# Optimization experiments

Hardware: AMD Instinct MI355X
Metric: run time of the kernel (lower is better)

The kernel has to match this reference:

```python
import jax, jax.numpy as jnp
import numpy as np

EMBED_DIM = 1024
NUM_HEADS = 16
HEAD_DIM = EMBED_DIM // NUM_HEADS
SCALE = HEAD_DIM ** -0.5


def setup_inputs() -> dict:
    key = jax.random.key(0)
    k_x, k_qkv, k_w, k_b = jax.random.split(key, 4)
    B, N = 2, 2048
    x = jax.random.normal(k_x, (B, N, EMBED_DIM), dtype=jnp.float32)
    # nn.Linear weights stored as (out, in); init with small normal
    w_qkv = jax.random.normal(k_qkv, (3 * EMBED_DIM, EMBED_DIM), dtype=jnp.float32) * (EMBED_DIM ** -0.5)
    w_out = jax.random.normal(k_w, (EMBED_DIM, EMBED_DIM), dtype=jnp.float32) * (EMBED_DIM ** -0.5)
    b_out = jax.random.normal(k_b, (EMBED_DIM,), dtype=jnp.float32) * 0.02
    return {"x": x, "w_qkv": w_qkv, "w_out": w_out, "b_out": b_out}


def reference(x, w_qkv, w_out, b_out):
    B, N, _ = x.shape
    # qkv: (B, N, 3*E) -> (B, N, 3, H, Dh)
    qkv = jnp.einsum('bne,fe->bnf', x, w_qkv).reshape(B, N, 3, NUM_HEADS, HEAD_DIM)
    q, k, v = qkv[:, :, 0], qkv[:, :, 1], qkv[:, :, 2]
    scores = jnp.einsum('bnhd,bmhd->bhnm', q, k) * SCALE
    attn = jax.nn.softmax(scores, axis=-1)  # dropout is identity in eval mode
    out = jnp.einsum('bhnm,bmhd->bnhd', attn, v).reshape(B, N, EMBED_DIM)
    return jnp.einsum('bne,fe->bnf', out, w_out) + b_out
```

## Files before the change

### kernel.cpp

```cpp
#include <hip/hip_runtime.h>
#include <stdint.h>
#include <stddef.h>

#define SEQ   2048
#define BATCH 2
#define NTOK  (SEQ*BATCH)
#define EMB   1024
#define QKVN  3072
#define NH    16
#define HD    64

typedef __bf16 bf16x8 __attribute__((ext_vector_type(8)));
typedef float  f32x4  __attribute__((ext_vector_type(4)));

__device__ __forceinline__ unsigned short f2b(float f) {
  union { float f; uint32_t u; } v; v.f = f;
  uint32_t r = v.u + 0x7fffu + ((v.u >> 16) & 1u);
  return (unsigned short)(r >> 16);
}

#define GLOAD_LDS16(gp, lp)                                                    \
  __builtin_amdgcn_global_load_lds(                                            \
      (__attribute__((address_space(1))) void*)(gp),                           \
      (__attribute__((address_space(3))) void*)(lp), 16, 0, 0)

__global__ void cvt3_kernel(const float* __restrict__ x,
                            const float* __restrict__ wq,
                            const float* __restrict__ wo,
                            unsigned short* __restrict__ xb,
                            unsigned short* __restrict__ wqb,
                            unsigned short* __restrict__ wob) {
  int i = blockIdx.x * blockDim.x + threadIdx.x;
  const float* in; unsigned short* out; int k;
  if (i < 1048576)              { in = x;  out = xb;  k = i; }
  else if (i < 1048576+786432)  { in = wq; out = wqb; k = i - 1048576; }
  else                          { in = wo; out = wob; k = i - (1048576+786432); }
  float4 v = ((const float4*)in)[k];
  ushort4 o;
  o.x = f2b(v.x); o.y = f2b(v.y); o.z = f2b(v.z); o.w = f2b(v.w);
  ((ushort4*)out)[k] = o;
}

__global__ __launch_bounds__(256) void gemm_bt(
    const unsigned short* __restrict__ A,
    const unsigned short* __restrict__ B,
    unsigned short* __restrict__ Cb,
    float* __restrict__ Cf,
    const float* __restrict__ bias,
    unsigned short* __restrict__ vt,
    int M, int N, int K, int mode)
{
  __shared__ unsigned short As[128*64];
  __shared__ unsigned short Bs[128*64];

  const int tid  = threadIdx.x;
  const int wave = tid >> 6, lane = tid & 63;
  const int l16  = lane & 15, quad = lane >> 4;
  const int tm = blockIdx.x * 128, tn = blockIdx.y * 128;
  const int wm = (wave & 1) * 64,  wn = (wave >> 1) * 64;

  f32x4 acc[4][4] = {};

  for (int k0 = 0; k0 < K; k0 += 64) {
    __syncthreads();
#pragma unroll
    for (int j = 0; j < 4; ++j) {
      const int p   = (wave*4 + j)*64 + lane;
      const int row = p >> 3;
      const int c   = ((p & 7) ^ (row & 7)) << 3;
      GLOAD_LDS16(A + (size_t)(tm + row)*K + (k0 + c), As + (wave*4 + j)*512);
      GLOAD_LDS16(B + (size_t)(tn + row)*K + (k0 + c), Bs + (wave*4 + j)*512);
    }
    __syncthreads();

#pragma unroll
    for (int ks = 0; ks < 2; ++ks) {
      bf16x8 af[4], bf[4];
#pragma unroll
      for (int i = 0; i < 4; ++i) {
        const int ca = ((ks*4 + quad) ^ (l16 & 7)) << 3;
        af[i] = *(const bf16x8*)(As + (wm + i*16 + l16)*64 + ca);
        bf[i] = *(const bf16x8*)(Bs + (wn + i*16 + l16)*64 + ca);
      }
#pragma unroll
      for (int mi = 0; mi < 4; ++mi)
#pragma unroll
        for (int ni = 0; ni < 4; ++ni)
          acc[mi][ni] = __builtin_amdgcn_mfma_f32_16x16x32_bf16(af[mi], bf[ni], acc[mi][ni], 0, 0, 0);
    }
  }

  if (mode == 1) {
#pragma unroll
    for (int mi = 0; mi < 4; ++mi)
#pragma unroll
      for (int ni = 0; ni < 4; ++ni)
#pragma unroll
        for (int r = 0; r < 4; ++r) {
          const int row = tm + wm + mi*16 + quad*4 + r;
          const int col = tn + wn + ni*16 + l16;
          Cf[(size_t)row*N + col] = acc[mi][ni][r] + bias[col];
        }
  } else {
    if (tn < 2048) {
#pragma unroll
      for (int mi = 0; mi < 4; ++mi)
#pragma unroll
        for (int ni = 0; ni < 4; ++ni)
#pragma unroll
          for (int r = 0; r < 4; ++r) {
            const int row = tm + wm + mi*16 + quad*4 + r;
            const int col = tn + wn + ni*16 + l16;
            Cb[(size_t)row*2048 + col] = f2b(acc[mi][ni][r]);
          }
    } else {
#pragma unroll
      for (int mi = 0; mi < 4; ++mi)
#pragma unroll
        for (int ni = 0; ni < 4; ++ni) {
          const int f    = tn + wn + ni*16 + l16 - 2048;
          const int row0 = tm + wm + mi*16 + quad*4;
          const int bb   = row0 >> 11;
          const int n0   = row0 & 2047;
          ushort4 pv;
          pv.x = f2b(acc[mi][ni][0]); pv.y = f2b(acc[mi][ni][1]);
          pv.z = f2b(acc[mi][ni][2]); pv.w = f2b(acc[mi][ni][3]);
          *(ushort4*)(vt + ((size_t)(bb*1024 + f))*2048 + n0) = pv;
        }
    }
  }
}

__global__ __launch_bounds__(256) void attn_kernel(
    const unsigned short* __restrict__ qk,
    const unsigned short* __restrict__ vT,
    unsigned short* __restrict__ aout)
{
  __shared__ unsigned short Ks[2][64*64];
  __shared__ unsigned short Vt[2][64*64];
  __shared__ unsigned short Pl[4*16*64];

  const int tid  = threadIdx.x;
  const int wave = tid >> 6, lane = tid & 63;
  const int l16  = lane & 15, quad = lane >> 4;

  const int flat = blockIdx.x;
  const int xcd  = flat & 7;
  const int idx  = flat >> 3;
  const int bh   = xcd*4 + (idx >> 5);
  const int qt   = idx & 31;
  const int b  = bh >> 4, h = bh & 15;
  const size_t tok0 = (size_t)b * SEQ;
  const int qrow0 = qt*64 + wave*16;
  const int swz = (l16 & 7) << 3;

  const int sp0  = wave*64 + lane;
  const int sp1  = 256 + wave*64 + lane;
  const int srow0 = sp0 >> 3, sc0 = ((sp0 & 7) ^ (srow0 & 7)) << 3;
  const int srow1 = sp1 >> 3, sc1 = ((sp1 & 7) ^ (srow1 & 7)) << 3;
  const unsigned short* kbase = qk + tok0*2048 + 1024 + h*64;
  const unsigned short* vbase = vT + ((size_t)(b*1024 + h*64))*2048;
  const int ldst0 = (wave*64)*8;
  const int ldst1 = (256 + wave*64)*8;

#define STAGE(dst, kk0s)                                                      \
  do {                                                                        \
    GLOAD_LDS16(kbase + (size_t)((kk0s) + srow0)*2048 + sc0, Ks[dst] + ldst0);\
    GLOAD_LDS16(vbase + (size_t)srow0*2048 + (kk0s) + sc0,   Vt[dst] + ldst0);\
    GLOAD_LDS16(kbase + (size_t)((kk0s) + srow1)*2048 + sc1, Ks[dst] + ldst1);\
    GLOAD_LDS16(vbase + (size_t)srow1*2048 + (kk0s) + sc1,   Vt[dst] + ldst1);\
  } while (0)

  bf16x8 qf[2];
  {
    const unsigned short* qp = qk + (tok0 + qrow0 + l16)*2048 + h*64;
#pragma unroll
    for (int ks = 0; ks < 2; ++ks) {
      bf16x8 t = *(const bf16x8*)(qp + ks*32 + quad*8);
#pragma unroll
      for (int j = 0; j < 8; ++j) t[j] = (__bf16)((float)t[j] * 0.125f);
      qf[ks] = t;
    }
  }

  f32x4 oacc[4] = {};
  float l_run = 0.f;
  unsigned short* Pw = Pl + wave*(16*64);
  const float LOG2E = 1.44269504f;
  const float OFF2  = 17.3123405f;

  STAGE(0, 0);
  __syncthreads();

  for (int kb = 0; kb < SEQ/64; ++kb) {
    const int cur = kb & 1;
    if (kb + 1 < SEQ/64) STAGE(cur ^ 1, (kb + 1)*64);

    const unsigned short* Kc = Ks[cur];
    const unsigned short* Vc = Vt[cur];

    f32x4 s[4] = {};
    __builtin_amdgcn_s_setprio(1);
#pragma unroll
    for (int ks = 0; ks < 2; ++ks)
#pragma unroll
      for (int mf = 0; mf < 4; ++mf) {
        bf16x8 kf = *(const bf16x8*)(Kc + (mf*16 + l16)*64 + (((ks*4 + quad) ^ (l16 & 7)) << 3));
        s[mf] = __builtin_amdgcn_mfma_f32_16x16x32_bf16(kf, qf[ks], s[mf], 0, 0, 0);
      }
    __builtin_amdgcn_s_setprio(0);

    {
      float rs = l_run;
#pragma unroll
      for (int mf = 0; mf < 4; ++mf) {
        union { float f; uint32_t u; } a0, a1, a2, a3;
        a0.f = __builtin_amdgcn_exp2f(fmaf(s[mf][0], LOG2E, -OFF2));
        a1.f = __builtin_amdgcn_exp2f(fmaf(s[mf][1], LOG2E, -OFF2));
        a2.f = __builtin_amdgcn_exp2f(fmaf(s[mf][2], LOG2E, -OFF2));
        a3.f = __builtin_amdgcn_exp2f(fmaf(s[mf][3], LOG2E, -OFF2));
        rs += (a0.f + a1.f) + (a2.f + a3.f);
        uint2 pk;
        pk.x = __builtin_amdgcn_perm(a1.u, a0.u, 0x07060302u);
        pk.y = __builtin_amdgcn_perm(a3.u, a2.u, 0x07060302u);
        *(uint2*)(Pw + l16*64 + ((mf*16 + quad*4) ^ swz)) = pk;
      }
      l_run = rs;
    }

    __builtin_amdgcn_s_setprio(1);
#pragma unroll
    for (int ks = 0; ks < 2; ++ks) {
      bf16x8 pf = *(const bf16x8*)(Pw + l16*64 + ((ks*32 + quad*8) ^ swz));
#pragma unroll
      for (int mf = 0; mf < 4; ++mf) {
        bf16x8 vf = *(const bf16x8*)(Vc + (mf*16 + l16)*64 + (((ks*4 + quad) ^ (l16 & 7)) << 3));
        oacc[mf] = __builtin_amdgcn_mfma_f32_16x16x32_bf16(vf, pf, oacc[mf], 0, 0, 0);
      }
    }
    __builtin_amdgcn_s_setprio(0);

    __syncthreads();
  }
#undef STAGE

  {
    float l = l_run;
    l += __shfl_xor(l, 16);
    l += __shfl_xor(l, 32);
    const float inv = 1.0f / l;
    const size_t trow = tok0 + qrow0 + l16;
#pragma unroll
    for (int mf = 0; mf < 4; ++mf) {
      ushort4 ov;
      ov.x = f2b(oacc[mf][0] * inv);
      ov.y = f2b(oacc[mf][1] * inv);
      ov.z = f2b(oacc[mf][2] * inv);
      ov.w = f2b(oacc[mf][3] * inv);
      *(ushort4*)(aout + trow*EMB + h*64 + mf*16 + quad*4) = ov;
    }
  }
}

extern "C" void kernel_launch(void* const* d_in, const int* in_sizes, int n_in,
                              void* d_out, int out_size, void* d_ws, size_t ws_size,
                              hipStream_t stream) {
  const float* x     = (const float*)d_in[0];
  const float* w_qkv = (const float*)d_in[1];
  const float* w_out = (const float*)d_in[2];
  const float* b_out = (const float*)d_in[3];

  char* ws = (char*)d_ws;
  unsigned short* xb    = (unsigned short*)(ws);
  unsigned short* wqkvb = (unsigned short*)(ws + 8388608);
  unsigned short* woutb = (unsigned short*)(ws + 14680064);
  unsigned short* qkb   = (unsigned short*)(ws + 16777216);
  unsigned short* vTb   = (unsigned short*)(ws + 33554432);
  unsigned short* aob   = (unsigned short*)(ws + 41943040);

  cvt3_kernel<<<8192, 256, 0, stream>>>(x, w_qkv, w_out, xb, wqkvb, woutb);

  gemm_bt<<<dim3(NTOK/128, QKVN/128), 256, 0, stream>>>(
      xb, wqkvb, qkb, nullptr, nullptr, vTb, NTOK, QKVN, EMB, 2);

  attn_kernel<<<dim3(1024), 256, 0, stream>>>(qkb, vTb, aob);

  gemm_bt<<<dim3(NTOK/128, EMB/128), 256, 0, stream>>>(
      aob, woutb, nullptr, (float*)d_out, b_out, nullptr, NTOK, EMB, EMB, 1);
}
```

Before: 205.1 us.

## Split attention KV tiles into 32-key sub-tiles with 4-deep LDS ring

The attention loop now stages K and V in 32-key sub-tiles across a four-slot LDS ring, prefetching two sub-tiles ahead instead of one 64-key tile. Each iteration computes both sub-tiles' QK^T first, then interleaves the exp/P-write and PV MFMAs per sub-tile, with new swizzles for the narrower V and P buffers. The goal is to overlap softmax VALU work with matrix ops and to issue loads further ahead. It adds more complex indexing, and the ring reuse relies on the existing barrier placement to stay correct.

```diff
diff --git a/kernel.cpp b/kernel.cpp
--- a/kernel.cpp
+++ b/kernel.cpp
@@ -136,9 +136,9 @@
     const unsigned short* __restrict__ vT,
     unsigned short* __restrict__ aout)
 {
-  __shared__ unsigned short Ks[2][64*64];
-  __shared__ unsigned short Vt[2][64*64];
-  __shared__ unsigned short Pl[4*16*64];
+  __shared__ unsigned short Ks[4][32*64];
+  __shared__ unsigned short Vt[4][64*32];
+  __shared__ unsigned short Pl[4*2*16*32];
 
   const int tid  = threadIdx.x;
   const int wave = tid >> 6, lane = tid & 63;
@@ -152,23 +152,23 @@
   const int b  = bh >> 4, h = bh & 15;
   const size_t tok0 = (size_t)b * SEQ;
   const int qrow0 = qt*64 + wave*16;
-  const int swz = (l16 & 7) << 3;
-
-  const int sp0  = wave*64 + lane;
-  const int sp1  = 256 + wave*64 + lane;
-  const int srow0 = sp0 >> 3, sc0 = ((sp0 & 7) ^ (srow0 & 7)) << 3;
-  const int srow1 = sp1 >> 3, sc1 = ((sp1 & 7) ^ (srow1 & 7)) << 3;
+  const int ksw = l16 & 7;
+  const int xsw = (l16 >> 1) & 3;
+
+  const int p     = wave*64 + lane;
+  const int krow  = p >> 3;
+  const int kc    = ((p & 7) ^ (krow & 7)) << 3;
+  const int vd    = p >> 2;
+  const int vc    = ((p & 3) ^ ((vd >> 1) & 3)) << 3;
   const unsigned short* kbase = qk + tok0*2048 + 1024 + h*64;
   const unsigned short* vbase = vT + ((size_t)(b*1024 + h*64))*2048;
-  const int ldst0 = (wave*64)*8;
-  const int ldst1 = (256 + wave*64)*8;
-
-#define STAGE(dst, kk0s)                                                      \
+  const int ldstw = wave*512;
+
+#define STAGE(bf, t)                                                          \
   do {                                                                        \
-    GLOAD_LDS16(kbase + (size_t)((kk0s) + srow0)*2048 + sc0, Ks[dst] + ldst0);\
-    GLOAD_LDS16(vbase + (size_t)srow0*2048 + (kk0s) + sc0,   Vt[dst] + ldst0);\
-    GLOAD_LDS16(kbase + (size_t)((kk0s) + srow1)*2048 + sc1, Ks[dst] + ldst1);\
-    GLOAD_LDS16(vbase + (size_t)srow1*2048 + (kk0s) + sc1,   Vt[dst] + ldst1);\
+    const int _kk = (t)*32;                                                   \
+    GLOAD_LDS16(kbase + (size_t)(_kk + krow)*2048 + kc, &Ks[bf][ldstw]);      \
+    GLOAD_LDS16(vbase + (size_t)vd*2048 + _kk + vc,     &Vt[bf][ldstw]);      \
   } while (0)
 
   bf16x8 qf[2];
@@ -185,56 +185,90 @@
 
   f32x4 oacc[4] = {};
   float l_run = 0.f;
-  unsigned short* Pw = Pl + wave*(16*64);
+  unsigned short* Pw0 = Pl + (wave*2 + 0)*512;
+  unsigned short* Pw1 = Pl + (wave*2 + 1)*512;
   const float LOG2E = 1.44269504f;
   const float OFF2  = 17.3123405f;
 
   STAGE(0, 0);
+  STAGE(1, 1);
   __syncthreads();
 
-  for (int kb = 0; kb < SEQ/64; ++kb) {
-    const int cur = kb & 1;
-    if (kb + 1 < SEQ/64) STAGE(cur ^ 1, (kb + 1)*64);
-
-    const unsigned short* Kc = Ks[cur];
-    const unsigned short* Vc = Vt[cur];
-
-    f32x4 s[4] = {};
+#pragma unroll 2
+  for (int kbb = 0; kbb < SEQ/64; ++kbb) {
+    const int t0 = kbb*2;
+    const int b0 = t0 & 3, b1 = (t0 + 1) & 3;
+    if (t0 + 2 < SEQ/32) { STAGE((t0+2)&3, t0+2); STAGE((t0+3)&3, t0+3); }
+
+    f32x4 sA[2] = {}, sB[2] = {};
     __builtin_amdgcn_s_setprio(1);
 #pragma unroll
     for (int ks = 0; ks < 2; ++ks)
 #pragma unroll
-      for (int mf = 0; mf < 4; ++mf) {
-        bf16x8 kf = *(const bf16x8*)(Kc + (mf*16 + l16)*64 + (((ks*4 + quad) ^ (l16 & 7)) << 3));
-        s[mf] = __builtin_amdgcn_mfma_f32_16x16x32_bf16(kf, qf[ks], s[mf], 0, 0, 0);
+      for (int mf = 0; mf < 2; ++mf) {
+        bf16x8 kf = *(const bf16x8*)(&Ks[b0][(mf*16 + l16)*64 + (((ks*4 + quad) ^ ksw) << 3)]);
+        sA[mf] = __builtin_amdgcn_mfma_f32_16x16x32_bf16(kf, qf[ks], sA[mf], 0, 0, 0);
+      }
+#pragma unroll
+    for (int ks = 0; ks < 2; ++ks)
+#pragma unroll
+      for (int mf = 0; mf < 2; ++mf) {
+        bf16x8 kf = *(const bf16x8*)(&Ks[b1][(mf*16 + l16)*64 + (((ks*4 + quad) ^ ksw) << 3)]);
+        sB[mf] = __builtin_amdgcn_mfma_f32_16x16x32_bf16(kf, qf[ks], sB[mf], 0, 0, 0);
       }
     __builtin_amdgcn_s_setprio(0);
 
     {
       float rs = l_run;
 #pragma unroll
-      for (int mf = 0; mf < 4; ++mf) {
+      for (int mf = 0; mf < 2; ++mf) {
         union { float f; uint32_t u; } a0, a1, a2, a3;
-        a0.f = __builtin_amdgcn_exp2f(fmaf(s[mf][0], LOG2E, -OFF2));
-        a1.f = __builtin_amdgcn_exp2f(fmaf(s[mf][1], LOG2E, -OFF2));
-        a2.f = __builtin_amdgcn_exp2f(fmaf(s[mf][2], LOG2E, -OFF2));
-        a3.f = __builtin_amdgcn_exp2f(fmaf(s[mf][3], LOG2E, -OFF2));
+        a0.f = __builtin_amdgcn_exp2f(fmaf(sA[mf][0], LOG2E, -OFF2));
+        a1.f = __builtin_amdgcn_exp2f(fmaf(sA[mf][1], LOG2E, -OFF2));
+        a2.f = __builtin_amdgcn_exp2f(fmaf(sA[mf][2], LOG2E, -OFF2));
+        a3.f = __builtin_amdgcn_exp2f(fmaf(sA[mf][3], LOG2E, -OFF2));
         rs += (a0.f + a1.f) + (a2.f + a3.f);
         uint2 pk;
         pk.x = __builtin_amdgcn_perm(a1.u, a0.u, 0x07060302u);
         pk.y = __builtin_amdgcn_perm(a3.u, a2.u, 0x07060302u);
-        *(uint2*)(Pw + l16*64 + ((mf*16 + quad*4) ^ swz)) = pk;
+        *(uint2*)(Pw0 + l16*32 + ((((mf*2 + (quad>>1)) ^ xsw) << 3) + (quad&1)*4)) = pk;
       }
       l_run = rs;
     }
-
     __builtin_amdgcn_s_setprio(1);
-#pragma unroll
-    for (int ks = 0; ks < 2; ++ks) {
-      bf16x8 pf = *(const bf16x8*)(Pw + l16*64 + ((ks*32 + quad*8) ^ swz));
+    {
+      bf16x8 pf = *(const bf16x8*)(Pw0 + l16*32 + ((quad ^ xsw) << 3));
 #pragma unroll
       for (int mf = 0; mf < 4; ++mf) {
-        bf16x8 vf = *(const bf16x8*)(Vc + (mf*16 + l16)*64 + (((ks*4 + quad) ^ (l16 & 7)) << 3));
+        bf16x8 vf = *(const bf16x8*)(&Vt[b0][(mf*16 + l16)*32 + ((quad ^ xsw) << 3)]);
+        oacc[mf] = __builtin_amdgcn_mfma_f32_16x16x32_bf16(vf, pf, oacc[mf], 0, 0, 0);
+      }
+    }
+    __builtin_amdgcn_s_setprio(0);
+
+    {
+      float rs = l_run;
+#pragma unroll
+      for (int mf = 0; mf < 2; ++mf) {
+        union { float f; uint32_t u; } a0, a1, a2, a3;
+        a0.f = __builtin_amdgcn_exp2f(fmaf(sB[mf][0], LOG2E, -OFF2));
+        a1.f = __builtin_amdgcn_exp2f(fmaf(sB[mf][1], LOG2E, -OFF2));
+        a2.f = __builtin_amdgcn_exp2f(fmaf(sB[mf][2], LOG2E, -OFF2));
+        a3.f = __builtin_amdgcn_exp2f(fmaf(sB[mf][3], LOG2E, -OFF2));
+        rs += (a0.f + a1.f) + (a2.f + a3.f);
+        uint2 pk;
+        pk.x = __builtin_amdgcn_perm(a1.u, a0.u, 0x07060302u);
+        pk.y = __builtin_amdgcn_perm(a3.u, a2.u, 0x07060302u);
+        *(uint2*)(Pw1 + l16*32 + ((((mf*2 + (quad>>1)) ^ xsw) << 3) + (quad&1)*4)) = pk;
+      }
+      l_run = rs;
+    }
+    __builtin_amdgcn_s_setprio(1);
+    {
+      bf16x8 pf = *(const bf16x8*)(Pw1 + l16*32 + ((quad ^ xsw) << 3));
+#pragma unroll
+      for (int mf = 0; mf < 4; ++mf) {
+        bf16x8 vf = *(const bf16x8*)(&Vt[b1][(mf*16 + l16)*32 + ((quad ^ xsw) << 3)]);
         oacc[mf] = __builtin_amdgcn_mfma_f32_16x16x32_bf16(vf, pf, oacc[mf], 0, 0, 0);
       }
     }
```

New measurement: 199.4 us. -2.8%, faster.
